# Kernel tuning notes

Hardware: AMD Instinct MI355X
Metric: run time of the kernel (lower is better)

Reference implementation:

```python
import jax, jax.numpy as jnp
import numpy as np

B, T, SLATE, D = 256, 16, 20, 256
N_ITEMS, N_USERS = 100000, 10000


def setup_inputs() -> dict:
    key = jax.random.key(0)
    ks = jax.random.split(key, 8)
    s = 1.0 / np.sqrt(D)  # PyTorch GRU/Linear init scale ~ U(-1/sqrt(H), 1/sqrt(H))
    return {
        "item_idxs": jax.random.randint(ks[0], (B, T, SLATE), 0, N_ITEMS),
        "user_idxs": jax.random.randint(ks[1], (B, T), 0, N_USERS),
        "responses": jnp.zeros((B, T, SLATE), jnp.float32),
        "item_table": jax.random.normal(ks[2], (N_ITEMS, D), jnp.float32) * 0.02,
        "user_table": jax.random.normal(ks[3], (N_USERS, D), jnp.float32) * 0.02,
        "W_ih": jax.random.uniform(ks[4], (3 * D, 2 * D), jnp.float32, -s, s),
        "W_hh": jax.random.uniform(ks[5], (3 * D, D), jnp.float32, -s, s),
        "b_ih": jnp.zeros((3 * D,), jnp.float32),
        "b_hh": jnp.zeros((3 * D,), jnp.float32),
        "W_out": jax.random.uniform(ks[6], (1, D), jnp.float32, -s, s),
        "b_out": jnp.zeros((1,), jnp.float32),
    }


def _gru_cell(x, h, W_ih, W_hh, b_ih, b_hh):
    # PyTorch GRUCell math. x: [N, 2D], h: [N, D]
    gi = x @ W_ih.T + b_ih  # [N, 3D]
    gh = h @ W_hh.T + b_hh  # [N, 3D]
    i_r, i_z, i_n = jnp.split(gi, 3, axis=-1)
    h_r, h_z, h_n = jnp.split(gh, 3, axis=-1)
    r = jax.nn.sigmoid(i_r + h_r)
    z = jax.nn.sigmoid(i_z + h_z)
    n = jnp.tanh(i_n + r * h_n)
    return (1.0 - z) * n + z * h


def reference(item_idxs, user_idxs, responses, item_table, user_table,
              W_ih, W_hh, b_ih, b_hh, W_out, b_out):
    # embedding lookup: item_embs [B,T,S,D], user_embs [B,T,D]
    item_embs = item_table[item_idxs]
    user_embs = user_table[user_idxs]
    N = B * T
    e = item_embs.reshape(N, SLATE, D).transpose(1, 0, 2)  # [S, N, D]
    h0 = user_embs.reshape(N, D)
    m0 = jnp.ones((N, 1), item_embs.dtype)  # 'soft' readout multiplier, 1 at step 0

    def step(carry, e_i):
        h, m = carry
        x = jnp.concatenate([e_i, e_i * m], axis=-1)  # [N, 2D]
        h = _gru_cell(x, h, W_ih, W_hh, b_ih, b_hh)
        y = h @ W_out.T + b_out  # [N, 1]
        return (h, jax.nn.sigmoid(y)), y[:, 0]

    _, ys = jax.lax.scan(step, (h0, m0), e)  # ys: [S, N]
    return ys.transpose(1, 0).reshape(B, T, SLATE)
```

## Files before the change

### kernel.cpp

```cpp
#include <hip/hip_runtime.h>
#include <math.h>

#define SLATE 20
#define DD 256
#define NSEQ 4096

typedef __attribute__((ext_vector_type(8))) short bf16x8;
typedef __attribute__((ext_vector_type(4))) float f32x4;
typedef unsigned short u16;
typedef unsigned int u32;

__device__ __forceinline__ u16 f2bf(float f) {
    unsigned u = __float_as_uint(f);
    u += 0x7fff + ((u >> 16) & 1);
    return (u16)(u >> 16);
}
__device__ __forceinline__ float blo(u32 u) { return __uint_as_float(u << 16); }
__device__ __forceinline__ float bhi(u32 u) { return __uint_as_float(u & 0xffff0000u); }
__device__ __forceinline__ float sigm_(float x) {
    return __builtin_amdgcn_rcpf(1.f + __builtin_amdgcn_exp2f(-1.44269504f * x));
}
__device__ __forceinline__ float tanh_(float x) {
    return 1.f - 2.f * __builtin_amdgcn_rcpf(1.f + __builtin_amdgcn_exp2f(2.88539008f * x));
}

__device__ __forceinline__ void gl_lds16(const void* g, void* l) {
    __builtin_amdgcn_global_load_lds(
        (const __attribute__((address_space(1))) unsigned int*)g,
        (__attribute__((address_space(3))) unsigned int*)l, 16, 0, 0);
}

__global__ void prep_w(const float* __restrict__ W_ih, const float* __restrict__ W_hh,
                       u16* __restrict__ W12, u16* __restrict__ Whh) {
    int i = blockIdx.x * 256 + threadIdx.x;
    if (i < 1536 * 256) {
        int j = i >> 8, k = i & 255;
        float v = (j < 768) ? W_ih[(size_t)j * 512 + k]
                            : W_ih[(size_t)(j - 768) * 512 + 256 + k];
        W12[i] = f2bf(v);
    } else {
        int i2 = i - 1536 * 256;
        Whh[i2] = f2bf(W_hh[i2]);
    }
}

__global__ void gather_e(int s0, const int* __restrict__ idxs, const float* __restrict__ itab,
                         u16* __restrict__ e_bf) {
    int g = blockIdx.x * 256 + threadIdx.x;
    int row = g >> 6, c = g & 63;
    int n = row & (NSEQ - 1), s = s0 + (row >> 12);
    int idx = idxs[n * SLATE + s];
    float4 v = *(const float4*)&itab[(size_t)idx * DD + c * 4];
    ushort4 o;
    o.x = f2bf(v.x); o.y = f2bf(v.y); o.z = f2bf(v.z); o.w = f2bf(v.w);
    *(ushort4*)&e_bf[(size_t)row * DD + c * 4] = o;
}

__global__ __launch_bounds__(256, 4) void gemm_e(
        const u16* __restrict__ e_bf, const u16* __restrict__ W12,
        const float* __restrict__ b_ih, const float* __restrict__ b_hh,
        u16* __restrict__ Ge) {
    __shared__ u16 A_s[128][32];
    __shared__ u16 B_s[128][32];

    const int tid = threadIdx.x;
    const int w = tid >> 6, l = tid & 63, lm = l & 15, lq = l >> 4;
    const int wm = w & 1, wn = w >> 1;
    const size_t m0 = (size_t)blockIdx.y * 128;
    const size_t n0 = (size_t)blockIdx.x * 128;

    f32x4 acc[4][4];
    f32x4 zero4 = {0.f, 0.f, 0.f, 0.f};
#pragma unroll
    for (int mi = 0; mi < 4; ++mi)
#pragma unroll
        for (int nj = 0; nj < 4; ++nj) acc[mi][nj] = zero4;

    const int srow = w * 16 + (l >> 2);
    const int skc = (l & 3) * 8;
    const u16* gA = e_bf + (m0 + srow) * DD + skc;
    const u16* gB = W12 + (n0 + srow) * DD + skc;
    u16* lA = &A_s[0][0] + w * 512 + l * 8;
    u16* lB = &B_s[0][0] + w * 512 + l * 8;

    for (int kt = 0; kt < 8; ++kt) {
        const int ko = kt * 32;
        gl_lds16(gA + ko, lA);
        gl_lds16(gA + 64 * DD + ko, lA + 2048);
        gl_lds16(gB + ko, lB);
        gl_lds16(gB + 64 * DD + ko, lB + 2048);
        __syncthreads();
        bf16x8 af[4], bfr[4];
#pragma unroll
        for (int mi = 0; mi < 4; ++mi)
            af[mi] = *(const bf16x8*)&A_s[wm * 64 + mi * 16 + lm][lq * 8];
#pragma unroll
        for (int nj = 0; nj < 4; ++nj)
            bfr[nj] = *(const bf16x8*)&B_s[wn * 64 + nj * 16 + lm][lq * 8];
#pragma unroll
        for (int nj = 0; nj < 4; ++nj)
#pragma unroll
            for (int mi = 0; mi < 4; ++mi)
                acc[mi][nj] = __builtin_amdgcn_mfma_f32_16x16x32_bf16(af[mi], bfr[nj], acc[mi][nj], 0, 0, 0);
        __syncthreads();
    }
    float bb[4];
#pragma unroll
    for (int nj = 0; nj < 4; ++nj) {
        int col = (int)n0 + wn * 64 + nj * 16 + lm;
        bb[nj] = 0.f;
        if (col < 768) bb[nj] = b_ih[col] + (col < 512 ? b_hh[col] : 0.f);
    }
#pragma unroll
    for (int mi = 0; mi < 4; ++mi)
#pragma unroll
        for (int rr = 0; rr < 4; ++rr) {
            u16* gp = Ge + (m0 + wm * 64 + mi * 16 + lq * 4 + rr) * 1536 + n0 + wn * 64 + lm;
#pragma unroll
            for (int nj = 0; nj < 4; ++nj) gp[nj * 16] = f2bf(acc[mi][nj][rr] + bb[nj]);
        }
}

__device__ __forceinline__ int hA_off(int seq, int kt, int lq2) {
    int v = ((kt & 3) << 2) | lq2;
    return kt * 512 + lq2 * 128 + ((seq ^ v) << 3);
}

__global__ __launch_bounds__(512, 2) void seq_kernel(
        int s0, int C,
        const u16* __restrict__ Ge,
        const u16* __restrict__ Whh,
        const int* __restrict__ user_idxs, const float* __restrict__ user_table,
        const float* __restrict__ b_hh,
        const float* __restrict__ W_out, const float* __restrict__ b_out,
        float* __restrict__ h_g, float* __restrict__ m_g, float* __restrict__ out)
{
    __shared__ u16   hA[4096];
    __shared__ float gh_s[16][770];
    __shared__ u16   geL[2][16][1536];

    const int tid = threadIdx.x;
    const int w = tid >> 6, l = tid & 63, lm = l & 15, lq = l >> 4;
    const int l5 = l & 31, sh = l >> 5;
    const int n0 = blockIdx.x * 16;
    const int sloc = 2 * w + sh;
    const int nw = n0 + sloc;
    const int jw2 = w * 96;

    bf16x8 warr[6][8];
    const u16* wb = Whh + (size_t)(jw2 + lm) * DD + lq * 8;
#pragma unroll
    for (int fi = 0; fi < 6; ++fi)
#pragma unroll
        for (int kt = 0; kt < 8; ++kt)
            warr[fi][kt] = *(const bf16x8*)(wb + fi * 16 * DD + kt * 32);

    float bn[6];
#pragma unroll
    for (int fi = 0; fi < 6; ++fi) {
        int colb = jw2 + fi * 16;
        bn[fi] = (colb >= 512) ? b_hh[colb + lm] : 0.f;
    }

    float wo[8];
#pragma unroll
    for (int j = 0; j < 4; ++j) {
        float2 t = *(const float2*)&W_out[2 * l5 + 64 * j];
        wo[2 * j] = t.x; wo[2 * j + 1] = t.y;
    }
    const float bo = b_out[0];

    float h_reg[8]; float m_w;
    if (s0 == 0) {
        const float* hu = user_table + (size_t)user_idxs[nw] * DD;
#pragma unroll
        for (int j = 0; j < 4; ++j) {
            float2 t = *(const float2*)&hu[2 * l5 + 64 * j];
            h_reg[2 * j] = t.x; h_reg[2 * j + 1] = t.y;
        }
        m_w = 1.f;
    } else {
        const float* hp = h_g + (size_t)nw * DD;
#pragma unroll
        for (int j = 0; j < 4; ++j) {
            float2 t = *(const float2*)&hp[2 * l5 + 64 * j];
            h_reg[2 * j] = t.x; h_reg[2 * j + 1] = t.y;
        }
        m_w = m_g[nw];
    }
#pragma unroll
    for (int j = 0; j < 4; ++j) {
        int ktw = (l5 >> 4) + 2 * j, lq2 = (l5 & 15) >> 2;
        u32 pk = (u32)f2bf(h_reg[2 * j]) | ((u32)f2bf(h_reg[2 * j + 1]) << 16);
        *(u32*)&hA[hA_off(sloc, ktw, lq2) + 2 * (l5 & 3)] = pk;
    }

    {
        const u16* g0 = Ge + (size_t)n0 * 1536;
        u16* l0 = &geL[0][0][0];
#pragma unroll
        for (int i = 0; i < 6; ++i)
            gl_lds16(g0 + tid * 8 + i * 4096, l0 + tid * 8 + i * 4096);
    }
    asm volatile("s_waitcnt lgkmcnt(0)" ::: "memory");
    __builtin_amdgcn_s_barrier();
    __builtin_amdgcn_sched_barrier(0);

    for (int sc = 0; sc < C; ++sc) {
        const int cur = sc & 1;

        if (sc + 1 < C) {
            const u16* gn = Ge + ((size_t)(sc + 1) * NSEQ + n0) * 1536;
            u16* ln = &geL[cur ^ 1][0][0];
#pragma unroll
            for (int i = 0; i < 6; ++i)
                gl_lds16(gn + tid * 8 + i * 4096, ln + tid * 8 + i * 4096);
        }
        __builtin_amdgcn_sched_barrier(0);

        f32x4 zero4 = {0.f, 0.f, 0.f, 0.f};
        f32x4 acc[6];
#pragma unroll
        for (int fi = 0; fi < 6; ++fi) acc[fi] = zero4;
#pragma unroll
        for (int kt = 0; kt < 8; ++kt) {
            bf16x8 af = *(const bf16x8*)&hA[hA_off(lm, kt, lq)];
#pragma unroll
            for (int fi = 0; fi < 6; ++fi)
                acc[fi] = __builtin_amdgcn_mfma_f32_16x16x32_bf16(af, warr[fi][kt], acc[fi], 0, 0, 0);
        }
#pragma unroll
        for (int fi = 0; fi < 6; ++fi)
#pragma unroll
            for (int rr = 0; rr < 4; ++rr)
                gh_s[lq * 4 + rr][jw2 + fi * 16 + lm] = acc[fi][rr] + bn[fi];

        if (sc + 1 < C) { asm volatile("s_waitcnt vmcnt(6) lgkmcnt(0)" ::: "memory"); }
        else            { asm volatile("s_waitcnt vmcnt(0) lgkmcnt(0)" ::: "memory"); }
        __builtin_amdgcn_s_barrier();
        __builtin_amdgcn_sched_barrier(0);

        const u32* grow = (const u32*)&geL[cur][sloc][0];
        float yv = 0.f;
#pragma unroll
        for (int j = 0; j < 4; ++j) {
            u32 g1r = grow[      l5 + 32 * j];
            u32 g1z = grow[128 + l5 + 32 * j];
            u32 g1n = grow[256 + l5 + 32 * j];
            u32 g2r = grow[384 + l5 + 32 * j];
            u32 g2z = grow[512 + l5 + 32 * j];
            u32 g2n = grow[640 + l5 + 32 * j];
            const int d0 = 2 * l5 + 64 * j;
            float2 ghr = *(const float2*)&gh_s[sloc][d0];
            float2 ghz = *(const float2*)&gh_s[sloc][256 + d0];
            float2 ghn = *(const float2*)&gh_s[sloc][512 + d0];
            float ir_lo = fmaf(m_w, blo(g2r), blo(g1r));
            float ir_hi = fmaf(m_w, bhi(g2r), bhi(g1r));
            float iz_lo = fmaf(m_w, blo(g2z), blo(g1z));
            float iz_hi = fmaf(m_w, bhi(g2z), bhi(g1z));
            float in_lo = fmaf(m_w, blo(g2n), blo(g1n));
            float in_hi = fmaf(m_w, bhi(g2n), bhi(g1n));
            float r_lo = sigm_(ir_lo + ghr.x);
            float r_hi = sigm_(ir_hi + ghr.y);
            float z_lo = sigm_(iz_lo + ghz.x);
            float z_hi = sigm_(iz_hi + ghz.y);
            float n_lo = tanh_(fmaf(r_lo, ghn.x, in_lo));
            float n_hi = tanh_(fmaf(r_hi, ghn.y, in_hi));
            float hn_lo = fmaf(z_lo, h_reg[2 * j] - n_lo, n_lo);
            float hn_hi = fmaf(z_hi, h_reg[2 * j + 1] - n_hi, n_hi);
            h_reg[2 * j] = hn_lo; h_reg[2 * j + 1] = hn_hi;
            int ktw = (l5 >> 4) + 2 * j, lq2 = (l5 & 15) >> 2;
            u32 pk = (u32)f2bf(hn_lo) | ((u32)f2bf(hn_hi) << 16);
            *(u32*)&hA[hA_off(sloc, ktw, lq2) + 2 * (l5 & 3)] = pk;
            yv += hn_lo * wo[2 * j] + hn_hi * wo[2 * j + 1];
        }
#pragma unroll
        for (int off = 16; off > 0; off >>= 1) yv += __shfl_xor(yv, off, 32);
        float y = yv + bo;
        if (l5 == 0) out[(size_t)nw * SLATE + (s0 + sc)] = y;
        m_w = sigm_(y);

        asm volatile("s_waitcnt lgkmcnt(0)" ::: "memory");
        __builtin_amdgcn_s_barrier();
        __builtin_amdgcn_sched_barrier(0);
    }

#pragma unroll
    for (int j = 0; j < 4; ++j) {
        float2 v; v.x = h_reg[2 * j]; v.y = h_reg[2 * j + 1];
        *(float2*)&h_g[(size_t)nw * DD + 2 * l5 + 64 * j] = v;
    }
    if (l5 == 0) m_g[nw] = m_w;
}

extern "C" void kernel_launch(void* const* d_in, const int* in_sizes, int n_in,
                              void* d_out, int out_size, void* d_ws, size_t ws_size,
                              hipStream_t stream) {
    const int*   item_idxs  = (const int*)d_in[0];
    const int*   user_idxs  = (const int*)d_in[1];
    const float* item_table = (const float*)d_in[3];
    const float* user_table = (const float*)d_in[4];
    const float* W_ih       = (const float*)d_in[5];
    const float* W_hh       = (const float*)d_in[6];
    const float* b_ih       = (const float*)d_in[7];
    const float* b_hh       = (const float*)d_in[8];
    const float* W_out      = (const float*)d_in[9];
    const float* b_out      = (const float*)d_in[10];
    float* out = (float*)d_out;

    const size_t fixed = 786432ull + 393216ull + 4194304ull + 16384ull;
    static const int cands[5] = {10, 5, 4, 2, 1};
    int C = 1;
    for (int i = 0; i < 5; ++i) {
        size_t need = (size_t)cands[i] * (12582912ull + 2097152ull) + fixed;
        if (need <= ws_size) { C = cands[i]; break; }
    }

    u16*   Ge   = (u16*)d_ws;
    u16*   e_bf = (u16*)((char*)d_ws + (size_t)C * 12582912ull);
    u16*   W12  = (u16*)((char*)e_bf + (size_t)C * 2097152ull);
    u16*   Whh  = (u16*)((char*)W12 + 786432ull);
    float* h_g  = (float*)((char*)Whh + 393216ull);
    float* m_g  = (float*)((char*)h_g + 4194304ull);

    prep_w<<<2304, 256, 0, stream>>>(W_ih, W_hh, W12, Whh);

    for (int s0 = 0; s0 < SLATE; s0 += C) {
        gather_e<<<C * 1024, 256, 0, stream>>>(s0, item_idxs, item_table, e_bf);
        dim3 gg(12, 32 * C);
        gemm_e<<<gg, 256, 0, stream>>>(e_bf, W12, b_ih, b_hh, Ge);
        seq_kernel<<<256, 512, 0, stream>>>(s0, C, Ge, Whh, user_idxs, user_table,
                                            b_hh, W_out, b_out, h_g, m_g, out);
    }
}
```

Baseline: 396.5 us.

## Prefetch per-step input gates into registers instead of LDS double-buffer

Drops the LDS double buffer for the precomputed input-gate activations (Ge). Each lane now loads its own slice straight into registers two steps ahead, using two register buffers and a loop unrolled by two. This frees about 96KB of LDS and removes the async global-to-LDS copies and their vmcnt waits. The cost is 48 extra VGPRs per thread under launch_bounds(512,2) alongside the resident weight fragments, which may cause spills, and the loads are no longer waited on explicitly.

```diff
diff --git a/kernel.cpp b/kernel.cpp
--- a/kernel.cpp
+++ b/kernel.cpp
@@ -137,7 +137,6 @@
 {
     __shared__ u16   hA[4096];
     __shared__ float gh_s[16][770];
-    __shared__ u16   geL[2][16][1536];
 
     const int tid = threadIdx.x;
     const int w = tid >> 6, l = tid & 63, lm = l & 15, lq = l >> 4;
@@ -195,95 +194,85 @@
         *(u32*)&hA[hA_off(sloc, ktw, lq2) + 2 * (l5 & 3)] = pk;
     }
 
-    {
-        const u16* g0 = Ge + (size_t)n0 * 1536;
-        u16* l0 = &geL[0][0][0];
-#pragma unroll
-        for (int i = 0; i < 6; ++i)
-            gl_lds16(g0 + tid * 8 + i * 4096, l0 + tid * 8 + i * 4096);
-    }
+    const u32* geBase = (const u32*)Ge + (size_t)nw * 768;
+    u32 geA[24], geB[24];
+
+#define GE_ISSUE(BUF, STP) do {                                               \
+        const u32* _b = geBase + (size_t)(STP) * (NSEQ * 768ull);             \
+        _Pragma("unroll") for (int _g = 0; _g < 6; ++_g)                      \
+        _Pragma("unroll") for (int _j = 0; _j < 4; ++_j)                      \
+            BUF[_g * 4 + _j] = _b[_g * 128 + _j * 32 + l5];                   \
+    } while (0)
+
+    GE_ISSUE(geA, 0);
+    if (C > 1) GE_ISSUE(geB, 1);
+    __builtin_amdgcn_sched_barrier(0);
+
     asm volatile("s_waitcnt lgkmcnt(0)" ::: "memory");
     __builtin_amdgcn_s_barrier();
     __builtin_amdgcn_sched_barrier(0);
 
-    for (int sc = 0; sc < C; ++sc) {
-        const int cur = sc & 1;
-
-        if (sc + 1 < C) {
-            const u16* gn = Ge + ((size_t)(sc + 1) * NSEQ + n0) * 1536;
-            u16* ln = &geL[cur ^ 1][0][0];
-#pragma unroll
-            for (int i = 0; i < 6; ++i)
-                gl_lds16(gn + tid * 8 + i * 4096, ln + tid * 8 + i * 4096);
-        }
-        __builtin_amdgcn_sched_barrier(0);
-
-        f32x4 zero4 = {0.f, 0.f, 0.f, 0.f};
-        f32x4 acc[6];
-#pragma unroll
-        for (int fi = 0; fi < 6; ++fi) acc[fi] = zero4;
-#pragma unroll
-        for (int kt = 0; kt < 8; ++kt) {
-            bf16x8 af = *(const bf16x8*)&hA[hA_off(lm, kt, lq)];
-#pragma unroll
-            for (int fi = 0; fi < 6; ++fi)
-                acc[fi] = __builtin_amdgcn_mfma_f32_16x16x32_bf16(af, warr[fi][kt], acc[fi], 0, 0, 0);
-        }
-#pragma unroll
-        for (int fi = 0; fi < 6; ++fi)
-#pragma unroll
-            for (int rr = 0; rr < 4; ++rr)
-                gh_s[lq * 4 + rr][jw2 + fi * 16 + lm] = acc[fi][rr] + bn[fi];
-
-        if (sc + 1 < C) { asm volatile("s_waitcnt vmcnt(6) lgkmcnt(0)" ::: "memory"); }
-        else            { asm volatile("s_waitcnt vmcnt(0) lgkmcnt(0)" ::: "memory"); }
-        __builtin_amdgcn_s_barrier();
-        __builtin_amdgcn_sched_barrier(0);
-
-        const u32* grow = (const u32*)&geL[cur][sloc][0];
-        float yv = 0.f;
-#pragma unroll
-        for (int j = 0; j < 4; ++j) {
-            u32 g1r = grow[      l5 + 32 * j];
-            u32 g1z = grow[128 + l5 + 32 * j];
-            u32 g1n = grow[256 + l5 + 32 * j];
-            u32 g2r = grow[384 + l5 + 32 * j];
-            u32 g2z = grow[512 + l5 + 32 * j];
-            u32 g2n = grow[640 + l5 + 32 * j];
-            const int d0 = 2 * l5 + 64 * j;
-            float2 ghr = *(const float2*)&gh_s[sloc][d0];
-            float2 ghz = *(const float2*)&gh_s[sloc][256 + d0];
-            float2 ghn = *(const float2*)&gh_s[sloc][512 + d0];
-            float ir_lo = fmaf(m_w, blo(g2r), blo(g1r));
-            float ir_hi = fmaf(m_w, bhi(g2r), bhi(g1r));
-            float iz_lo = fmaf(m_w, blo(g2z), blo(g1z));
-            float iz_hi = fmaf(m_w, bhi(g2z), bhi(g1z));
-            float in_lo = fmaf(m_w, blo(g2n), blo(g1n));
-            float in_hi = fmaf(m_w, bhi(g2n), bhi(g1n));
-            float r_lo = sigm_(ir_lo + ghr.x);
-            float r_hi = sigm_(ir_hi + ghr.y);
-            float z_lo = sigm_(iz_lo + ghz.x);
-            float z_hi = sigm_(iz_hi + ghz.y);
-            float n_lo = tanh_(fmaf(r_lo, ghn.x, in_lo));
-            float n_hi = tanh_(fmaf(r_hi, ghn.y, in_hi));
-            float hn_lo = fmaf(z_lo, h_reg[2 * j] - n_lo, n_lo);
-            float hn_hi = fmaf(z_hi, h_reg[2 * j + 1] - n_hi, n_hi);
-            h_reg[2 * j] = hn_lo; h_reg[2 * j + 1] = hn_hi;
-            int ktw = (l5 >> 4) + 2 * j, lq2 = (l5 & 15) >> 2;
-            u32 pk = (u32)f2bf(hn_lo) | ((u32)f2bf(hn_hi) << 16);
-            *(u32*)&hA[hA_off(sloc, ktw, lq2) + 2 * (l5 & 3)] = pk;
-            yv += hn_lo * wo[2 * j] + hn_hi * wo[2 * j + 1];
-        }
-#pragma unroll
-        for (int off = 16; off > 0; off >>= 1) yv += __shfl_xor(yv, off, 32);
-        float y = yv + bo;
-        if (l5 == 0) out[(size_t)nw * SLATE + (s0 + sc)] = y;
-        m_w = sigm_(y);
-
-        asm volatile("s_waitcnt lgkmcnt(0)" ::: "memory");
-        __builtin_amdgcn_s_barrier();
-        __builtin_amdgcn_sched_barrier(0);
-    }
+#define SEQ_STEP(BUF, SC) {                                                   \
+        f32x4 zero4 = {0.f, 0.f, 0.f, 0.f};                                   \
+        f32x4 acc[6];                                                         \
+        _Pragma("unroll") for (int fi = 0; fi < 6; ++fi) acc[fi] = zero4;     \
+        _Pragma("unroll") for (int kt = 0; kt < 8; ++kt) {                    \
+            bf16x8 af = *(const bf16x8*)&hA[hA_off(lm, kt, lq)];              \
+            _Pragma("unroll") for (int fi = 0; fi < 6; ++fi)                  \
+                acc[fi] = __builtin_amdgcn_mfma_f32_16x16x32_bf16(af, warr[fi][kt], acc[fi], 0, 0, 0); \
+        }                                                                     \
+        _Pragma("unroll") for (int fi = 0; fi < 6; ++fi)                      \
+        _Pragma("unroll") for (int rr = 0; rr < 4; ++rr)                      \
+            gh_s[lq * 4 + rr][jw2 + fi * 16 + lm] = acc[fi][rr] + bn[fi];     \
+        asm volatile("s_waitcnt lgkmcnt(0)" ::: "memory");                    \
+        __builtin_amdgcn_s_barrier();                                         \
+        __builtin_amdgcn_sched_barrier(0);                                    \
+        float yv = 0.f;                                                       \
+        _Pragma("unroll") for (int j = 0; j < 4; ++j) {                       \
+            u32 g1r = BUF[0 * 4 + j], g1z = BUF[1 * 4 + j], g1n = BUF[2 * 4 + j]; \
+            u32 g2r = BUF[3 * 4 + j], g2z = BUF[4 * 4 + j], g2n = BUF[5 * 4 + j]; \
+            const int d0 = 2 * l5 + 64 * j;                                   \
+            float2 ghr = *(const float2*)&gh_s[sloc][d0];                     \
+            float2 ghz = *(const float2*)&gh_s[sloc][256 + d0];               \
+            float2 ghn = *(const float2*)&gh_s[sloc][512 + d0];               \
+            float ir_lo = fmaf(m_w, blo(g2r), blo(g1r));                      \
+            float ir_hi = fmaf(m_w, bhi(g2r), bhi(g1r));                      \
+            float iz_lo = fmaf(m_w, blo(g2z), blo(g1z));                      \
+            float iz_hi = fmaf(m_w, bhi(g2z), bhi(g1z));                      \
+            float in_lo = fmaf(m_w, blo(g2n), blo(g1n));                      \
+            float in_hi = fmaf(m_w, bhi(g2n), bhi(g1n));                      \
+            float r_lo = sigm_(ir_lo + ghr.x);                                \
+            float r_hi = sigm_(ir_hi + ghr.y);                                \
+            float z_lo = sigm_(iz_lo + ghz.x);                                \
+            float z_hi = sigm_(iz_hi + ghz.y);                                \
+            float n_lo = tanh_(fmaf(r_lo, ghn.x, in_lo));                     \
+            float n_hi = tanh_(fmaf(r_hi, ghn.y, in_hi));                     \
+            float hn_lo = fmaf(z_lo, h_reg[2 * j] - n_lo, n_lo);              \
+            float hn_hi = fmaf(z_hi, h_reg[2 * j + 1] - n_hi, n_hi);          \
+            h_reg[2 * j] = hn_lo; h_reg[2 * j + 1] = hn_hi;                   \
+            int ktw = (l5 >> 4) + 2 * j, lq2 = (l5 & 15) >> 2;                \
+            u32 pk = (u32)f2bf(hn_lo) | ((u32)f2bf(hn_hi) << 16);             \
+            *(u32*)&hA[hA_off(sloc, ktw, lq2) + 2 * (l5 & 3)] = pk;           \
+            yv += hn_lo * wo[2 * j] + hn_hi * wo[2 * j + 1];                  \
+        }                                                                     \
+        if ((SC) + 2 < C) GE_ISSUE(BUF, (SC) + 2);                            \
+        __builtin_amdgcn_sched_barrier(0);                                    \
+        _Pragma("unroll") for (int off = 16; off > 0; off >>= 1)              \
+            yv += __shfl_xor(yv, off, 32);                                    \
+        float y = yv + bo;                                                    \
+        if (l5 == 0) out[(size_t)nw * SLATE + (s0 + (SC))] = y;               \
+        m_w = sigm_(y);                                                       \
+        asm volatile("s_waitcnt lgkmcnt(0)" ::: "memory");                    \
+        __builtin_amdgcn_s_barrier();                                         \
+        __builtin_amdgcn_sched_barrier(0);                                    \
+    }
+
+    for (int sc = 0; sc < C; sc += 2) {
+        SEQ_STEP(geA, sc);
+        if (sc + 1 < C) SEQ_STEP(geB, sc + 1);
+    }
+#undef SEQ_STEP
+#undef GE_ISSUE
 
 #pragma unroll
     for (int j = 0; j < 4; ++j) {
```

New measurement: 568.5 us. 1.43x slower.

## Fuse next-chunk embedding gather into GEMM kernel with double-buffered inputs

Applied to the files above, without the earlier changes.

The per-chunk gather kernel is replaced, for every chunk after the first, by extra blocks inside the gemm_e launch that gather the next chunk's item embeddings into a second buffer. One block in five does gather work and the rest do the GEMM tiles, using a 1-D grid remapped to tile coordinates. This removes a kernel launch per chunk and lets the memory-bound gather overlap with the compute-bound GEMM. The cost is a second embedding buffer in the workspace, which may force a smaller chunk count C, plus heavier block scheduling inside the GEMM.

```diff
diff --git a/kernel.cpp b/kernel.cpp
--- a/kernel.cpp
+++ b/kernel.cpp
@@ -59,15 +59,39 @@
 __global__ __launch_bounds__(256, 4) void gemm_e(
         const u16* __restrict__ e_bf, const u16* __restrict__ W12,
         const float* __restrict__ b_ih, const float* __restrict__ b_hh,
-        u16* __restrict__ Ge) {
+        u16* __restrict__ Ge,
+        int withGather, int s0n, int C,
+        const int* __restrict__ idxs, const float* __restrict__ itab,
+        u16* __restrict__ e_nxt) {
     __shared__ u16 A_s[128][32];
     __shared__ u16 B_s[128][32];
+
+    const int bid = blockIdx.x;
+    int gemm_ord = bid;
+    if (withGather) {
+        const int q = bid / 5, r = bid - q * 5;
+        if (r == 4) {
+            const int total = C * 262144;
+            const int GB = gridDim.x / 5;
+            for (int g = q * 256 + threadIdx.x; g < total; g += GB * 256) {
+                int row = g >> 6, c = g & 63;
+                int n = row & (NSEQ - 1), s = s0n + (row >> 12);
+                int idx = idxs[n * SLATE + s];
+                float4 v = *(const float4*)&itab[(size_t)idx * DD + c * 4];
+                ushort4 o;
+                o.x = f2bf(v.x); o.y = f2bf(v.y); o.z = f2bf(v.z); o.w = f2bf(v.w);
+                *(ushort4*)&e_nxt[(size_t)row * DD + c * 4] = o;
+            }
+            return;
+        }
+        gemm_ord = bid - q;
+    }
 
     const int tid = threadIdx.x;
     const int w = tid >> 6, l = tid & 63, lm = l & 15, lq = l >> 4;
     const int wm = w & 1, wn = w >> 1;
-    const size_t m0 = (size_t)blockIdx.y * 128;
-    const size_t n0 = (size_t)blockIdx.x * 128;
+    const size_t m0 = (size_t)(gemm_ord / 12) * 128;
+    const size_t n0 = (size_t)(gemm_ord % 12) * 128;
 
     f32x4 acc[4][4];
     f32x4 zero4 = {0.f, 0.f, 0.f, 0.f};
@@ -312,23 +336,33 @@
     static const int cands[5] = {10, 5, 4, 2, 1};
     int C = 1;
     for (int i = 0; i < 5; ++i) {
-        size_t need = (size_t)cands[i] * (12582912ull + 2097152ull) + fixed;
+        size_t need = (size_t)cands[i] * (12582912ull + 2ull * 2097152ull) + fixed;
         if (need <= ws_size) { C = cands[i]; break; }
     }
 
     u16*   Ge   = (u16*)d_ws;
-    u16*   e_bf = (u16*)((char*)d_ws + (size_t)C * 12582912ull);
-    u16*   W12  = (u16*)((char*)e_bf + (size_t)C * 2097152ull);
+    u16*   e_b0 = (u16*)((char*)d_ws + (size_t)C * 12582912ull);
+    u16*   e_b1 = (u16*)((char*)e_b0 + (size_t)C * 2097152ull);
+    u16*   W12  = (u16*)((char*)e_b1 + (size_t)C * 2097152ull);
     u16*   Whh  = (u16*)((char*)W12 + 786432ull);
     float* h_g  = (float*)((char*)Whh + 393216ull);
     float* m_g  = (float*)((char*)h_g + 4194304ull);
 
     prep_w<<<2304, 256, 0, stream>>>(W_ih, W_hh, W12, Whh);
 
-    for (int s0 = 0; s0 < SLATE; s0 += C) {
-        gather_e<<<C * 1024, 256, 0, stream>>>(s0, item_idxs, item_table, e_bf);
-        dim3 gg(12, 32 * C);
-        gemm_e<<<gg, 256, 0, stream>>>(e_bf, W12, b_ih, b_hh, Ge);
+    int ci = 0;
+    for (int s0 = 0; s0 < SLATE; s0 += C, ++ci) {
+        u16* eCur = (ci & 1) ? e_b1 : e_b0;
+        u16* eNxt = (ci & 1) ? e_b0 : e_b1;
+        const int wg = (s0 + C < SLATE) ? 1 : 0;
+
+        if (ci == 0)
+            gather_e<<<C * 1024, 256, 0, stream>>>(0, item_idxs, item_table, eCur);
+
+        const int grid = wg ? 480 * C : 384 * C;
+        gemm_e<<<grid, 256, 0, stream>>>(eCur, W12, b_ih, b_hh, Ge,
+                                         wg, s0 + C, C, item_idxs, item_table, eNxt);
+
         seq_kernel<<<256, 512, 0, stream>>>(s0, C, Ge, Whh, user_idxs, user_table,
                                             b_hh, W_out, b_out, h_g, m_g, out);
     }
```

Measured after the change: 413.1 us. +4.2%, slower.
